# Optimization experiments

Measured on AMD Instinct MI355X. Metric: run time of the kernel, lower is better.

The kernel has to match this reference:

```python
import jax, jax.numpy as jnp
import numpy as np

B, N, F, H, OUT, K, L = 32, 2048, 3, 64, 128, 16, 3


def _edge_mlp(e, w1, b1, wo, bo):
    # Faithful to the given MLP.forward: layer1 -> ReLU -> output (layer2 is skipped!)
    return jax.nn.relu(e @ w1 + b1) @ wo + bo


def _dynamic_edge_conv(x, k, w1, b1, wo, bo):
    # x: [B, N, D]. kNN in feature space (self included, distance 0), per graph.
    sq = jnp.sum(x * x, axis=-1)                                   # [B, N]
    d2 = sq[:, :, None] + sq[:, None, :] - 2.0 * jnp.einsum('bnd,bmd->bnm', x, x)
    _, idx = jax.lax.top_k(-d2, k)                                 # [B, N, K]
    x_j = jax.vmap(lambda xb, ib: xb[ib])(x, idx)                  # [B, N, K, D] gather
    x_i = jnp.broadcast_to(x[:, :, None, :], x_j.shape)
    e = jnp.concatenate([x_i, x_j - x_i], axis=-1)                 # EdgeConv message [B,N,K,2D]
    h = _edge_mlp(e, w1, b1, wo, bo)                               # [B, N, K, H]
    return jnp.mean(h, axis=2)                                     # aggr='mean' -> [B, N, H]


def setup_inputs() -> dict:
    key = jax.random.key(0)
    ks = jax.random.split(key, 20)
    inp = {'x': jax.random.normal(ks[0], (B, N, F), dtype=jnp.float32)}
    kit = iter(ks[1:])
    for i in range(L):
        din = 2 * F if i == 0 else 2 * H
        inp[f'w1_{i}'] = jax.random.normal(next(kit), (din, H), jnp.float32) / np.sqrt(din)
        inp[f'b1_{i}'] = jnp.zeros((H,), jnp.float32)
        inp[f'wo_{i}'] = jax.random.normal(next(kit), (H, H), jnp.float32) / np.sqrt(H)
        inp[f'bo_{i}'] = jnp.zeros((H,), jnp.float32)
    inp['fw1'] = jax.random.normal(next(kit), (H, H), jnp.float32) / np.sqrt(H)
    inp['fb1'] = jnp.zeros((H,), jnp.float32)
    inp['fw2'] = jax.random.normal(next(kit), (H, OUT), jnp.float32) / np.sqrt(H)
    inp['fb2'] = jnp.zeros((OUT,), jnp.float32)
    return inp


def reference(x, w1_0, b1_0, wo_0, bo_0, w1_1, b1_1, wo_1, bo_1, w1_2, b1_2, wo_2, bo_2, fw1, fb1, fw2, fb2):
    layers = [(w1_0, b1_0, wo_0, bo_0), (w1_1, b1_1, wo_1, bo_1), (w1_2, b1_2, wo_2, bo_2)]
    h = x
    for (w1, b1, wo, bo) in layers:
        h = _dynamic_edge_conv(h, K, w1, b1, wo, bo)
    g = jnp.mean(h, axis=1)                                        # global_mean_pool -> [B, H]
    return jax.nn.relu(g @ fw1 + fb1) @ fw2 + fb2                  # [B, OUT]
```

## Files before the change

kernel.cpp:

```cpp
#include <hip/hip_runtime.h>

#define BB 32
#define NN 2048
#define FF 3
#define HH 64
#define OUTC 128
#define KK 16
#define BN (BB * NN)

typedef __attribute__((ext_vector_type(8))) __bf16 bf16x8;
typedef __attribute__((ext_vector_type(4))) float f32x4;

__device__ __forceinline__ unsigned int packkey(float d2, unsigned int m) {
    unsigned int bb = __builtin_bit_cast(unsigned int, d2);
    unsigned int msk = (unsigned int)((int)bb >> 31);
    unsigned int srt = bb ^ (msk | 0x80000000u);
    return (srt & 0xFFFFF800u) | m;
}

__device__ __forceinline__ void ce(unsigned int& a, unsigned int& b) {
    unsigned int lo = a < b ? a : b;
    unsigned int hi = a < b ? b : a;
    a = lo; b = hi;
}

__device__ __forceinline__ void sort16(unsigned int k[16]) {
#pragma unroll
    for (int p = 1; p < 16; p <<= 1)
#pragma unroll
        for (int q = p; q >= 1; q >>= 1)
#pragma unroll
            for (int j = q % p; j + q < 16; j += 2 * q)
#pragma unroll
                for (int i = 0; i < q; ++i) {
                    int x = i + j, y = i + j + q;
                    if (y < 16 && (x / (2 * p) == y / (2 * p))) ce(k[x], k[y]);
                }
}

__device__ __forceinline__ void merge16(unsigned int keys[16], const unsigned int nk[16]) {
    unsigned int t[16];
#pragma unroll
    for (int i = 0; i < 16; ++i) {
        unsigned int b = nk[15 - i];
        t[i] = keys[i] < b ? keys[i] : b;
    }
#pragma unroll
    for (int d = 8; d >= 1; d >>= 1)
#pragma unroll
        for (int i = 0; i < 16; ++i)
            if ((i & d) == 0) ce(t[i], t[i ^ d]);
#pragma unroll
    for (int i = 0; i < 16; ++i) keys[i] = t[i];
}

__device__ __forceinline__ unsigned short bfbits(float v) {
    return __builtin_bit_cast(unsigned short, (__bf16)v);
}

__global__ __launch_bounds__(256) void pack3_kernel(const float* __restrict__ x,
                                                    const float* __restrict__ w1,
                                                    const float* __restrict__ b1,
                                                    float* __restrict__ P,
                                                    float* __restrict__ Q,
                                                    unsigned short* __restrict__ idx32) {
    __shared__ float4 lds_c[256];
    __shared__ unsigned int Km[64 * 68];
    const int tid = threadIdx.x;

    if (blockIdx.x >= 1024) {
        const int h = tid & 63;
        const int pl = tid >> 6;
        const long p = (long)(blockIdx.x - 1024) * 4 + pl;
        const float* fp = x + p * 3;
        const float fv[3] = {fp[0], fp[1], fp[2]};
        float accp = 0.f, accq = 0.f;
#pragma unroll
        for (int d = 0; d < 3; ++d) {
            float wa = w1[d * HH + h];
            float wb = w1[(3 + d) * HH + h];
            accp = fmaf(fv[d], wa - wb, accp);
            accq = fmaf(fv[d], wb, accq);
        }
        P[p * HH + h] = accp + b1[h];
        Q[p * HH + h] = accq;
        return;
    }

    const int xcd = blockIdx.x & 7;
    const int ii = blockIdx.x >> 3;
    const int b = xcd + 8 * (ii >> 5);
    const int rg = ii & 31;
    const long pbase = (long)b * NN;
    const int r = tid >> 2, slot = tid & 3;
    const int row = rg * 64 + r;

    const float* rp = x + (pbase + row) * 3;
    const float xr0 = rp[0], xr1 = rp[1], xr2 = rp[2];

    unsigned int keys[KK];
#pragma unroll
    for (int j = 0; j < KK; ++j) keys[j] = 0xFFFFFFFFu;

    float c0, c1, c2, c3;
    {
        const float* cp = x + (pbase + tid) * 3;
        c0 = cp[0]; c1 = cp[1]; c2 = cp[2];
        c3 = c0 * c0 + c1 * c1 + c2 * c2;
    }

    for (int t = 0; t < NN / 256; ++t) {
        __syncthreads();
        lds_c[tid] = make_float4(c0, c1, c2, c3);
        __syncthreads();
        if (t < NN / 256 - 1) {
            const int m = (t + 1) * 256 + tid;
            const float* cp = x + (pbase + m) * 3;
            c0 = cp[0]; c1 = cp[1]; c2 = cp[2];
            c3 = c0 * c0 + c1 * c1 + c2 * c2;
        }
        const int cbase = slot * 64;
#pragma unroll
        for (int bb = 0; bb < 4; ++bb) {
            unsigned int nk[16];
#pragma unroll
            for (int cc = 0; cc < 16; ++cc) {
                float4 v = lds_c[cbase + bb * 16 + cc];
                float dot = fmaf(xr0, v.x, fmaf(xr1, v.y, xr2 * v.z));
                float d2 = fmaf(-2.0f, dot, v.w);
                nk[cc] = packkey(d2, (unsigned int)(t * 256 + cbase + bb * 16 + cc));
            }
            sort16(nk);
            merge16(keys, nk);
        }
    }

    {
        uint4* kw = (uint4*)&Km[r * 68 + slot * 16];
#pragma unroll
        for (int q = 0; q < 4; ++q)
            kw[q] = make_uint4(keys[4 * q], keys[4 * q + 1], keys[4 * q + 2], keys[4 * q + 3]);
    }
    __syncthreads();
    if (slot < 2) {
        const unsigned int* k0 = &Km[r * 68 + slot * 32];
        const unsigned int* k1 = k0 + 16;
        unsigned short ms[16];
#pragma unroll
        for (int j = 0; j < 16; ++j) {
            unsigned int a = k0[j], bv = k1[15 - j];
            ms[j] = (unsigned short)((a < bv ? a : bv) & 0x7FFu);
        }
        uint4* op = (uint4*)(idx32 + ((pbase + row) * 32 + slot * 16));
        op[0] = ((const uint4*)ms)[0];
        op[1] = ((const uint4*)ms)[1];
    }
}

__global__ __launch_bounds__(256) void prep_pq64_kernel(const float* __restrict__ feat,
                                                        const float* __restrict__ w1,
                                                        const float* __restrict__ b1,
                                                        float* __restrict__ P,
                                                        float* __restrict__ Q,
                                                        float* __restrict__ sqo) {
    __shared__ float rows[64 * HH];
    const int tid = threadIdx.x;
    const int h = tid & 63;
    const int wv = tid >> 6;
    const long row0 = (long)blockIdx.x * 64;

    float wdiff[64], wbv[64];
#pragma unroll
    for (int d = 0; d < 64; ++d) {
        float wa = w1[d * HH + h];
        float wb_ = w1[(HH + d) * HH + h];
        wdiff[d] = wa - wb_;
        wbv[d] = wb_;
    }
    const float bv = b1[h];

    {
        const float4* src = (const float4*)(feat + row0 * HH);
        float4* dst = (float4*)rows;
#pragma unroll
        for (int i = 0; i < 4; ++i) dst[tid + 256 * i] = src[tid + 256 * i];
    }
    __syncthreads();

    for (int r = wv * 16; r < wv * 16 + 16; ++r) {
        const long p = row0 + r;
        if (sqo) {
            float fvh = rows[r * HH + h];
            float s = fvh * fvh;
            s += __shfl_xor(s, 1);
            s += __shfl_xor(s, 2);
            s += __shfl_xor(s, 4);
            s += __shfl_xor(s, 8);
            s += __shfl_xor(s, 16);
            s += __shfl_xor(s, 32);
            if (h == 0) sqo[p] = s;
        }
        float ap0 = 0.f, ap1 = 0.f, aq0 = 0.f, aq1 = 0.f;
#pragma unroll
        for (int d4 = 0; d4 < 16; ++d4) {
            float4 fv = *(const float4*)&rows[r * HH + d4 * 4];
            ap0 = fmaf(fv.x, wdiff[4 * d4 + 0], ap0);
            aq0 = fmaf(fv.x, wbv[4 * d4 + 0], aq0);
            ap1 = fmaf(fv.y, wdiff[4 * d4 + 1], ap1);
            aq1 = fmaf(fv.y, wbv[4 * d4 + 1], aq1);
            ap0 = fmaf(fv.z, wdiff[4 * d4 + 2], ap0);
            aq0 = fmaf(fv.z, wbv[4 * d4 + 2], aq0);
            ap1 = fmaf(fv.w, wdiff[4 * d4 + 3], ap1);
            aq1 = fmaf(fv.w, wbv[4 * d4 + 3], aq1);
        }
        P[p * HH + h] = (ap0 + ap1) + bv;
        Q[p * HH + h] = aq0 + aq1;
    }
}

#define APAD 80
#define DPAD 68

__global__ __launch_bounds__(256) void knn_filter_kernel(const float* __restrict__ feat,
                                                         const float* __restrict__ sq,
                                                         unsigned short* __restrict__ idx32) {
    __shared__ __align__(16) __bf16 Ab[64 * APAD];
    __shared__ __align__(16) __bf16 Bb[64 * APAD];
    __shared__ __align__(16) unsigned int Dt[64 * DPAD];
    __shared__ float SqC[64];

    const int tid = threadIdx.x;
    const int xcd = blockIdx.x & 7;
    const int ii = blockIdx.x >> 3;
    const int b = xcd + 8 * (ii >> 5);
    const int rg = ii & 31;
    const long pbase = (long)b * NN;
    const int row0 = rg * 64;

    {
        const float4* src = (const float4*)(feat + (pbase + row0) * 64);
#pragma unroll
        for (int it = 0; it < 4; ++it) {
            const int i = it * 256 + tid;
            float4 v = src[i];
            const int rw = i >> 4, col = (i & 15) * 4;
            unsigned short u[4] = {bfbits(v.x), bfbits(v.y), bfbits(v.z), bfbits(v.w)};
            *(uint2*)&Ab[rw * APAD + col] = *(const uint2*)u;
        }
    }
    __syncthreads();

    const int wv = tid >> 6, ln = tid & 63;
    const int n16 = ln & 15, quad = ln >> 4;
    bf16x8 af0, af1;
    {
        const __bf16* ap = &Ab[(wv * 16 + n16) * APAD + quad * 8];
        af0 = *(const bf16x8*)ap;
        af1 = *(const bf16x8*)(ap + 32);
    }

    const int r = tid >> 2, slot = tid & 3;
    unsigned int keys[KK];
#pragma unroll
    for (int j = 0; j < KK; ++j) keys[j] = 0xFFFFFFFFu;

    float4 pv[4];
    float psq;
    {
        const float4* src = (const float4*)(feat + pbase * 64);
#pragma unroll
        for (int it = 0; it < 4; ++it) pv[it] = src[it * 256 + tid];
        psq = (tid < 64) ? sq[pbase + tid] : 0.f;
    }

    for (int t = 0; t < NN / 64; ++t) {
#pragma unroll
        for (int it = 0; it < 4; ++it) {
            const int i = it * 256 + tid;
            const int rw = i >> 4, col = (i & 15) * 4;
            unsigned short u[4] = {bfbits(pv[it].x), bfbits(pv[it].y),
                                   bfbits(pv[it].z), bfbits(pv[it].w)};
            *(uint2*)&Bb[rw * APAD + col] = *(const uint2*)u;
        }
        if (tid < 64) SqC[tid] = psq;
        __syncthreads();

#pragma unroll
        for (int ct = 0; ct < 4; ++ct) {
            const __bf16* bp = &Bb[(ct * 16 + n16) * APAD + quad * 8];
            bf16x8 bf0 = *(const bf16x8*)bp;
            bf16x8 bf1 = *(const bf16x8*)(bp + 32);
            f32x4 acc = {0.f, 0.f, 0.f, 0.f};
            acc = __builtin_amdgcn_mfma_f32_16x16x32_bf16(af0, bf0, acc, 0, 0, 0);
            acc = __builtin_amdgcn_mfma_f32_16x16x32_bf16(af1, bf1, acc, 0, 0, 0);
            const int ccol = ct * 16 + n16;
            const float sqc = SqC[ccol];
            const unsigned int m = (unsigned int)(t * 64 + ccol);
#pragma unroll
            for (int rr = 0; rr < 4; ++rr) {
                const int rrow = wv * 16 + quad * 4 + rr;
                Dt[rrow * DPAD + ccol] = packkey(fmaf(-2.0f, acc[rr], sqc), m);
            }
        }
        __syncthreads();

        if (t < NN / 64 - 1) {
            const float4* src = (const float4*)(feat + (pbase + (long)(t + 1) * 64) * 64);
#pragma unroll
            for (int it = 0; it < 4; ++it) pv[it] = src[it * 256 + tid];
            if (tid < 64) psq = sq[pbase + (t + 1) * 64 + tid];
        }

        {
            const uint4* kp = (const uint4*)&Dt[r * DPAD + slot * 16];
            unsigned int nk[16];
#pragma unroll
            for (int q = 0; q < 4; ++q) {
                uint4 kv = kp[q];
                nk[4 * q + 0] = kv.x; nk[4 * q + 1] = kv.y;
                nk[4 * q + 2] = kv.z; nk[4 * q + 3] = kv.w;
            }
            sort16(nk);
            merge16(keys, nk);
        }
    }

    __syncthreads();
    {
        uint4* kw = (uint4*)&Dt[r * DPAD + slot * 16];
#pragma unroll
        for (int q = 0; q < 4; ++q)
            kw[q] = make_uint4(keys[4 * q], keys[4 * q + 1], keys[4 * q + 2], keys[4 * q + 3]);
    }
    __syncthreads();
    if (slot < 2) {
        const unsigned int* k0 = &Dt[r * DPAD + slot * 32];
        const unsigned int* k1 = k0 + 16;
        unsigned short ms[16];
#pragma unroll
        for (int j = 0; j < 16; ++j) {
            unsigned int a = k0[j], bv = k1[15 - j];
            ms[j] = (unsigned short)((a < bv ? a : bv) & 0x7FFu);
        }
        uint4* op = (uint4*)(idx32 + ((pbase + row0 + r) * 32 + slot * 16));
        op[0] = ((const uint4*)ms)[0];
        op[1] = ((const uint4*)ms)[1];
    }
}

__global__ __launch_bounds__(256) void rescore3_kernel(const float* __restrict__ x,
                                                       const unsigned short* __restrict__ idx32,
                                                       const float* __restrict__ P,
                                                       const float* __restrict__ Q,
                                                       const float* __restrict__ wo,
                                                       const float* __restrict__ bo,
                                                       float* __restrict__ outf,
                                                       float* __restrict__ sqn) {
    __shared__ float rowf[8][3];
    __shared__ float Sc[8][32];
    __shared__ int Ji[8][32];
    __shared__ int Li[8][KK];
    __shared__ float Rl[8][HH];
    const int tid = threadIdx.x;
    const int w = tid >> 6, ln = tid & 63;
    const int rw = ln >> 5, c = ln & 31;
    const int xcd = blockIdx.x & 7;
    const int ii = blockIdx.x >> 3;
    const int batch = xcd + 8 * (ii >> 8);
    const int rb = ii & 255;
    const long pbase = (long)batch * NN;
    const long pblk = pbase + (long)rb * 8;
    const long p = pblk + w * 2 + rw;
    const int row_ = w * 2 + rw;

    for (int i = tid; i < 24; i += 256) rowf[i / 3][i % 3] = x[pblk * 3 + i];
    Ji[row_][c] = (int)idx32[p * 32 + c];
    __syncthreads();

    {
        const int jj = Ji[row_][c];
        const float* cp = x + (pbase + jj) * 3;
        const float c0 = cp[0], c1 = cp[1], c2 = cp[2];
        const float sqc = c0 * c0 + c1 * c1 + c2 * c2;
        float dot = fmaf(rowf[row_][0], c0, fmaf(rowf[row_][1], c1, rowf[row_][2] * c2));
        Sc[row_][c] = fmaf(-2.0f, dot, sqc);
    }
    __syncthreads();

    {
        const float score = Sc[row_][c];
        const int j = Ji[row_][c];
        int rank = 0;
#pragma unroll
        for (int m = 0; m < 32; ++m) {
            float dm = Sc[row_][m];
            int jm = Ji[row_][m];
            rank += (dm < score || (dm == score && jm < j)) ? 1 : 0;
        }
        if (rank < KK) Li[row_][rank] = j;
    }
    __syncthreads();

    const int h = tid & 63, pl = tid >> 6;
#pragma unroll
    for (int rr0 = 0; rr0 < 2; ++rr0) {
        const int rr = pl + rr0 * 4;
        const long pp = pblk + rr;
        const float Pv = P[pp * HH + h];
        float acc = 0.f;
#pragma unroll
        for (int k = 0; k < KK; ++k) {
            int j2 = Li[rr][k];
            acc += fmaxf(Pv + Q[(pbase + j2) * HH + h], 0.f);
        }
        Rl[rr][h] = acc * (1.f / KK);
    }
    __syncthreads();
#pragma unroll
    for (int rr0 = 0; rr0 < 2; ++rr0) {
        const int rr = pl + rr0 * 4;
        float o = bo[h];
#pragma unroll
        for (int l = 0; l < HH; ++l) o = fmaf(Rl[rr][l], wo[l * HH + h], o);
        outf[(pblk + rr) * HH + h] = o;
        float s2 = o * o;
        s2 += __shfl_xor(s2, 1);
        s2 += __shfl_xor(s2, 2);
        s2 += __shfl_xor(s2, 4);
        s2 += __shfl_xor(s2, 8);
        s2 += __shfl_xor(s2, 16);
        s2 += __shfl_xor(s2, 32);
        if (h == 0) sqn[pblk + rr] = s2;
    }
}

__global__ __launch_bounds__(256) void rescore64_kernel(const float* __restrict__ feat,
                                                        const float* __restrict__ sq,
                                                        const unsigned short* __restrict__ idx32,
                                                        const float* __restrict__ P,
                                                        const float* __restrict__ Q,
                                                        const float* __restrict__ wo,
                                                        const float* __restrict__ bo,
                                                        float* __restrict__ outf) {
    __shared__ float rowf[8][HH];
    __shared__ float Sc[8][32];
    __shared__ int Ji[8][32];
    __shared__ float Sq32[8][32];
    __shared__ int Li[8][KK];
    __shared__ float Rl[8][HH];
    const int tid = threadIdx.x;
    const int w = tid >> 6, ln = tid & 63;
    const int rw = ln >> 5, c = ln & 31;
    const int xcd = blockIdx.x & 7;
    const int ii = blockIdx.x >> 3;
    const int batch = xcd + 8 * (ii >> 8);
    const int rb = ii & 255;
    const long pbase = (long)batch * NN;
    const long pblk = pbase + (long)rb * 8;
    const long p = pblk + w * 2 + rw;
    const int row_ = w * 2 + rw;

    for (int i = tid; i < 8 * HH; i += 256) rowf[i / HH][i % HH] = feat[pblk * HH + i];
    {
        const int j0 = (int)idx32[p * 32 + c];
        Ji[row_][c] = j0;
        Sq32[row_][c] = sq[pbase + j0];
    }
    __syncthreads();

    {
        const int cg = ln >> 2, e = ln & 3;
#pragma unroll
        for (int rr = 0; rr < 2; ++rr) {
#pragma unroll
            for (int pp = 0; pp < 2; ++pp) {
                const int row = w * 2 + rr;
                const int cand = pp * 16 + cg;
                const int jj = Ji[row][cand];
                const float* cb = feat + (pbase + jj) * 64;
                float part = 0.f;
#pragma unroll
                for (int blk = 0; blk < 4; ++blk) {
                    float4 cv = *(const float4*)(cb + blk * 16 + e * 4);
                    float4 rv = *(const float4*)&rowf[row][blk * 16 + e * 4];
                    part = fmaf(rv.x, cv.x, part);
                    part = fmaf(rv.y, cv.y, part);
                    part = fmaf(rv.z, cv.z, part);
                    part = fmaf(rv.w, cv.w, part);
                }
                part += __shfl_xor(part, 1);
                part += __shfl_xor(part, 2);
                if (e == 0) Sc[row][cand] = fmaf(-2.0f, part, Sq32[row][cand]);
            }
        }
    }
    __syncthreads();

    {
        const float score = Sc[row_][c];
        const int j = Ji[row_][c];
        int rank = 0;
#pragma unroll
        for (int m = 0; m < 32; ++m) {
            float dm = Sc[row_][m];
            int jm = Ji[row_][m];
            rank += (dm < score || (dm == score && jm < j)) ? 1 : 0;
        }
        if (rank < KK) Li[row_][rank] = j;
    }
    __syncthreads();

    const int h = tid & 63, pl = tid >> 6;
#pragma unroll
    for (int rr0 = 0; rr0 < 2; ++rr0) {
        const int rr = pl + rr0 * 4;
        const long pp = pblk + rr;
        const float Pv = P[pp * HH + h];
        float acc = 0.f;
#pragma unroll
        for (int k = 0; k < KK; ++k) {
            int j2 = Li[rr][k];
            acc += fmaxf(Pv + Q[(pbase + j2) * HH + h], 0.f);
        }
        Rl[rr][h] = acc * (1.f / KK);
    }
    __syncthreads();
#pragma unroll
    for (int rr0 = 0; rr0 < 2; ++rr0) {
        const int rr = pl + rr0 * 4;
        float o = bo[h];
#pragma unroll
        for (int l = 0; l < HH; ++l) o = fmaf(Rl[rr][l], wo[l * HH + h], o);
        outf[(pblk + rr) * HH + h] = o;
    }
}

__global__ __launch_bounds__(256) void pool_partial_kernel(const float* __restrict__ feat,
                                                           float* __restrict__ pp) {
    __shared__ float part[4][HH];
    const int batch = blockIdx.x >> 3;
    const int chk = blockIdx.x & 7;
    const int tid = threadIdx.x;
    const int h = tid & 63;
    const int sub = tid >> 6;
    float s = 0.f;
    const float* fp = feat + ((long)batch * NN + chk * 256 + sub * 64) * HH + h;
    for (int n = 0; n < 64; ++n) s += fp[(long)n * HH];
    part[sub][h] = s;
    __syncthreads();
    if (tid < HH)
        pp[(batch * 8 + chk) * HH + h] = part[0][h] + part[1][h] + part[2][h] + part[3][h];
}

__global__ __launch_bounds__(256) void head_kernel(const float* __restrict__ pp,
                                                   const float* __restrict__ fw1,
                                                   const float* __restrict__ fb1,
                                                   const float* __restrict__ fw2,
                                                   const float* __restrict__ fb2,
                                                   float* __restrict__ out) {
    __shared__ float g[HH];
    __shared__ float tl[HH];
    const int b = blockIdx.x;
    const int tid = threadIdx.x;
    if (tid < HH) {
        float s = 0.f;
#pragma unroll
        for (int c = 0; c < 8; ++c) s += pp[(b * 8 + c) * HH + tid];
        g[tid] = s * (1.f / NN);
    }
    __syncthreads();
    if (tid < HH) {
        float a = fb1[tid];
#pragma unroll
        for (int l = 0; l < HH; ++l) a = fmaf(g[l], fw1[l * HH + tid], a);
        tl[tid] = fmaxf(a, 0.f);
    }
    __syncthreads();
    if (tid < OUTC) {
        float o = fb2[tid];
#pragma unroll
        for (int l = 0; l < HH; ++l) o = fmaf(tl[l], fw2[l * OUTC + tid], o);
        out[(long)b * OUTC + tid] = o;
    }
}

extern "C" void kernel_launch(void* const* d_in, const int* in_sizes, int n_in,
                              void* d_out, int out_size, void* d_ws, size_t ws_size,
                              hipStream_t stream) {
    const float* x    = (const float*)d_in[0];
    const float* w1_0 = (const float*)d_in[1];
    const float* b1_0 = (const float*)d_in[2];
    const float* wo_0 = (const float*)d_in[3];
    const float* bo_0 = (const float*)d_in[4];
    const float* w1_1 = (const float*)d_in[5];
    const float* b1_1 = (const float*)d_in[6];
    const float* wo_1 = (const float*)d_in[7];
    const float* bo_1 = (const float*)d_in[8];
    const float* w1_2 = (const float*)d_in[9];
    const float* b1_2 = (const float*)d_in[10];
    const float* wo_2 = (const float*)d_in[11];
    const float* bo_2 = (const float*)d_in[12];
    const float* fw1  = (const float*)d_in[13];
    const float* fb1  = (const float*)d_in[14];
    const float* fw2  = (const float*)d_in[15];
    const float* fb2  = (const float*)d_in[16];
    float* out = (float*)d_out;

    float* featA = (float*)d_ws;
    float* featB = featA + (long)BN * HH;
    float* Pb    = featB + (long)BN * HH;
    float* Qb    = Pb + (long)BN * HH;
    float* sqA   = Qb + (long)BN * HH;
    float* sqB   = sqA + BN;
    unsigned short* idx32 = (unsigned short*)(sqB + BN);
    float* ppb   = (float*)(idx32 + (long)BN * 32);

    pack3_kernel<<<1024 + BN / 4, 256, 0, stream>>>(x, w1_0, b1_0, Pb, Qb, idx32);
    rescore3_kernel<<<BN / 8, 256, 0, stream>>>(x, idx32, Pb, Qb, wo_0, bo_0, featA, sqB);

    prep_pq64_kernel<<<BN / 64, 256, 0, stream>>>(featA, w1_1, b1_1, Pb, Qb, nullptr);
    knn_filter_kernel<<<BB * 32, 256, 0, stream>>>(featA, sqB, idx32);
    rescore64_kernel<<<BN / 8, 256, 0, stream>>>(featA, sqB, idx32, Pb, Qb, wo_1, bo_1, featB);

    prep_pq64_kernel<<<BN / 64, 256, 0, stream>>>(featB, w1_2, b1_2, Pb, Qb, sqA);
    knn_filter_kernel<<<BB * 32, 256, 0, stream>>>(featB, sqA, idx32);
    rescore64_kernel<<<BN / 8, 256, 0, stream>>>(featB, sqA, idx32, Pb, Qb, wo_2, bo_2, featA);

    pool_partial_kernel<<<BB * 8, 256, 0, stream>>>(featA, ppb);
    head_kernel<<<BB, 256, 0, stream>>>(ppb, fw1, fb1, fw2, fb2, out);
}
```

Measured before the change: 619.2 us.

## Merge P/Q prep into kNN filter launch and fold squared norms into rescore

The separate prep_pq64 and knn_filter kernels are merged into one launch of 2048 blocks. Blocks 0-1023 run the kNN filter and blocks 1024-2047 compute P/Q, sharing one union shared-memory buffer, so the two independent jobs overlap on the GPU and one launch plus its tail is removed. The squared-norm computation for the next layer moves out of prep and into the rescore epilogue, which avoids re-reading the features. Rescore also gets a min-blocks-per-SM launch bound and loads P early. In exchange, the union buffer makes every block reserve the larger shared-memory footprint, and the launch bound may increase register pressure.

```diff
diff --git a/kernel.cpp b/kernel.cpp
--- a/kernel.cpp
+++ b/kernel.cpp
@@ -157,79 +157,70 @@
     }
 }
 
-__global__ __launch_bounds__(256) void prep_pq64_kernel(const float* __restrict__ feat,
-                                                        const float* __restrict__ w1,
-                                                        const float* __restrict__ b1,
-                                                        float* __restrict__ P,
-                                                        float* __restrict__ Q,
-                                                        float* __restrict__ sqo) {
-    __shared__ float rows[64 * HH];
-    const int tid = threadIdx.x;
-    const int h = tid & 63;
-    const int wv = tid >> 6;
-    const long row0 = (long)blockIdx.x * 64;
-
-    float wdiff[64], wbv[64];
-#pragma unroll
-    for (int d = 0; d < 64; ++d) {
-        float wa = w1[d * HH + h];
-        float wb_ = w1[(HH + d) * HH + h];
-        wdiff[d] = wa - wb_;
-        wbv[d] = wb_;
-    }
-    const float bv = b1[h];
-
-    {
-        const float4* src = (const float4*)(feat + row0 * HH);
-        float4* dst = (float4*)rows;
-#pragma unroll
-        for (int i = 0; i < 4; ++i) dst[tid + 256 * i] = src[tid + 256 * i];
-    }
-    __syncthreads();
-
-    for (int r = wv * 16; r < wv * 16 + 16; ++r) {
-        const long p = row0 + r;
-        if (sqo) {
-            float fvh = rows[r * HH + h];
-            float s = fvh * fvh;
-            s += __shfl_xor(s, 1);
-            s += __shfl_xor(s, 2);
-            s += __shfl_xor(s, 4);
-            s += __shfl_xor(s, 8);
-            s += __shfl_xor(s, 16);
-            s += __shfl_xor(s, 32);
-            if (h == 0) sqo[p] = s;
-        }
-        float ap0 = 0.f, ap1 = 0.f, aq0 = 0.f, aq1 = 0.f;
-#pragma unroll
-        for (int d4 = 0; d4 < 16; ++d4) {
-            float4 fv = *(const float4*)&rows[r * HH + d4 * 4];
-            ap0 = fmaf(fv.x, wdiff[4 * d4 + 0], ap0);
-            aq0 = fmaf(fv.x, wbv[4 * d4 + 0], aq0);
-            ap1 = fmaf(fv.y, wdiff[4 * d4 + 1], ap1);
-            aq1 = fmaf(fv.y, wbv[4 * d4 + 1], aq1);
-            ap0 = fmaf(fv.z, wdiff[4 * d4 + 2], ap0);
-            aq0 = fmaf(fv.z, wbv[4 * d4 + 2], aq0);
-            ap1 = fmaf(fv.w, wdiff[4 * d4 + 3], ap1);
-            aq1 = fmaf(fv.w, wbv[4 * d4 + 3], aq1);
-        }
-        P[p * HH + h] = (ap0 + ap1) + bv;
-        Q[p * HH + h] = aq0 + aq1;
-    }
-}
-
 #define APAD 80
 #define DPAD 68
-
-__global__ __launch_bounds__(256) void knn_filter_kernel(const float* __restrict__ feat,
-                                                         const float* __restrict__ sq,
-                                                         unsigned short* __restrict__ idx32) {
-    __shared__ __align__(16) __bf16 Ab[64 * APAD];
-    __shared__ __align__(16) __bf16 Bb[64 * APAD];
-    __shared__ __align__(16) unsigned int Dt[64 * DPAD];
-    __shared__ float SqC[64];
-
+#define SMEM_U32 (38144 / 4)
+
+__global__ __launch_bounds__(256) void filter_prep64_kernel(const float* __restrict__ feat,
+                                                            const float* __restrict__ sq,
+                                                            const float* __restrict__ w1,
+                                                            const float* __restrict__ b1,
+                                                            float* __restrict__ P,
+                                                            float* __restrict__ Q,
+                                                            unsigned short* __restrict__ idx32) {
+    __shared__ __align__(16) unsigned int smem[SMEM_U32];
     const int tid = threadIdx.x;
+
+    if (blockIdx.x >= 1024) {
+        float* rows = (float*)smem;
+        const int h = tid & 63;
+        const int wv = tid >> 6;
+        const long row0 = (long)(blockIdx.x - 1024) * 64;
+
+        float wdiff[64], wbv[64];
+#pragma unroll
+        for (int d = 0; d < 64; ++d) {
+            float wa = w1[d * HH + h];
+            float wb_ = w1[(HH + d) * HH + h];
+            wdiff[d] = wa - wb_;
+            wbv[d] = wb_;
+        }
+        const float bv = b1[h];
+
+        {
+            const float4* src = (const float4*)(feat + row0 * HH);
+            float4* dst = (float4*)rows;
+#pragma unroll
+            for (int i = 0; i < 4; ++i) dst[tid + 256 * i] = src[tid + 256 * i];
+        }
+        __syncthreads();
+
+        for (int r = wv * 16; r < wv * 16 + 16; ++r) {
+            const long p = row0 + r;
+            float ap0 = 0.f, ap1 = 0.f, aq0 = 0.f, aq1 = 0.f;
+#pragma unroll
+            for (int d4 = 0; d4 < 16; ++d4) {
+                float4 fv = *(const float4*)&rows[r * HH + d4 * 4];
+                ap0 = fmaf(fv.x, wdiff[4 * d4 + 0], ap0);
+                aq0 = fmaf(fv.x, wbv[4 * d4 + 0], aq0);
+                ap1 = fmaf(fv.y, wdiff[4 * d4 + 1], ap1);
+                aq1 = fmaf(fv.y, wbv[4 * d4 + 1], aq1);
+                ap0 = fmaf(fv.z, wdiff[4 * d4 + 2], ap0);
+                aq0 = fmaf(fv.z, wbv[4 * d4 + 2], aq0);
+                ap1 = fmaf(fv.w, wdiff[4 * d4 + 3], ap1);
+                aq1 = fmaf(fv.w, wbv[4 * d4 + 3], aq1);
+            }
+            P[p * HH + h] = (ap0 + ap1) + bv;
+            Q[p * HH + h] = aq0 + aq1;
+        }
+        return;
+    }
+
+    __bf16* Ab = (__bf16*)smem;
+    __bf16* Bb = Ab + 64 * APAD;
+    unsigned int* Dt = (unsigned int*)(Bb + 64 * APAD);
+    float* SqC = (float*)(Dt + 64 * DPAD);
+
     const int xcd = blockIdx.x & 7;
     const int ii = blockIdx.x >> 3;
     const int b = xcd + 8 * (ii >> 5);
@@ -434,14 +425,15 @@
     }
 }
 
-__global__ __launch_bounds__(256) void rescore64_kernel(const float* __restrict__ feat,
-                                                        const float* __restrict__ sq,
-                                                        const unsigned short* __restrict__ idx32,
-                                                        const float* __restrict__ P,
-                                                        const float* __restrict__ Q,
-                                                        const float* __restrict__ wo,
-                                                        const float* __restrict__ bo,
-                                                        float* __restrict__ outf) {
+__global__ __launch_bounds__(256, 8) void rescore64_kernel(const float* __restrict__ feat,
+                                                           const float* __restrict__ sq,
+                                                           const unsigned short* __restrict__ idx32,
+                                                           const float* __restrict__ P,
+                                                           const float* __restrict__ Q,
+                                                           const float* __restrict__ wo,
+                                                           const float* __restrict__ bo,
+                                                           float* __restrict__ outf,
+                                                           float* __restrict__ sqn) {
     __shared__ float rowf[8][HH];
     __shared__ float Sc[8][32];
     __shared__ int Ji[8][32];
@@ -459,6 +451,10 @@
     const long pblk = pbase + (long)rb * 8;
     const long p = pblk + w * 2 + rw;
     const int row_ = w * 2 + rw;
+    const int h = tid & 63, pl = tid >> 6;
+
+    const float Pv0 = P[(pblk + pl) * HH + h];
+    const float Pv1 = P[(pblk + pl + 4) * HH + h];
 
     for (int i = tid; i < 8 * HH; i += 256) rowf[i / HH][i % HH] = feat[pblk * HH + i];
     {
@@ -510,12 +506,10 @@
     }
     __syncthreads();
 
-    const int h = tid & 63, pl = tid >> 6;
 #pragma unroll
     for (int rr0 = 0; rr0 < 2; ++rr0) {
         const int rr = pl + rr0 * 4;
-        const long pp = pblk + rr;
-        const float Pv = P[pp * HH + h];
+        const float Pv = rr0 ? Pv1 : Pv0;
         float acc = 0.f;
 #pragma unroll
         for (int k = 0; k < KK; ++k) {
@@ -532,6 +526,16 @@
 #pragma unroll
         for (int l = 0; l < HH; ++l) o = fmaf(Rl[rr][l], wo[l * HH + h], o);
         outf[(pblk + rr) * HH + h] = o;
+        if (sqn) {
+            float s2 = o * o;
+            s2 += __shfl_xor(s2, 1);
+            s2 += __shfl_xor(s2, 2);
+            s2 += __shfl_xor(s2, 4);
+            s2 += __shfl_xor(s2, 8);
+            s2 += __shfl_xor(s2, 16);
+            s2 += __shfl_xor(s2, 32);
+            if (h == 0) sqn[pblk + rr] = s2;
+        }
     }
 }
 
@@ -618,13 +622,13 @@
     pack3_kernel<<<1024 + BN / 4, 256, 0, stream>>>(x, w1_0, b1_0, Pb, Qb, idx32);
     rescore3_kernel<<<BN / 8, 256, 0, stream>>>(x, idx32, Pb, Qb, wo_0, bo_0, featA, sqB);
 
-    prep_pq64_kernel<<<BN / 64, 256, 0, stream>>>(featA, w1_1, b1_1, Pb, Qb, nullptr);
-    knn_filter_kernel<<<BB * 32, 256, 0, stream>>>(featA, sqB, idx32);
-    rescore64_kernel<<<BN / 8, 256, 0, stream>>>(featA, sqB, idx32, Pb, Qb, wo_1, bo_1, featB);
-
-    prep_pq64_kernel<<<BN / 64, 256, 0, stream>>>(featB, w1_2, b1_2, Pb, Qb, sqA);
-    knn_filter_kernel<<<BB * 32, 256, 0, stream>>>(featB, sqA, idx32);
-    rescore64_kernel<<<BN / 8, 256, 0, stream>>>(featB, sqA, idx32, Pb, Qb, wo_2, bo_2, featA);
+    filter_prep64_kernel<<<2048, 256, 0, stream>>>(featA, sqB, w1_1, b1_1, Pb, Qb, idx32);
+    rescore64_kernel<<<BN / 8, 256, 0, stream>>>(featA, sqB, idx32, Pb, Qb, wo_1, bo_1,
+                                                 featB, sqA);
+
+    filter_prep64_kernel<<<2048, 256, 0, stream>>>(featB, sqA, w1_2, b1_2, Pb, Qb, idx32);
+    rescore64_kernel<<<BN / 8, 256, 0, stream>>>(featB, sqA, idx32, Pb, Qb, wo_2, bo_2,
+                                                 featA, nullptr);
 
     pool_partial_kernel<<<BB * 8, 256, 0, stream>>>(featA, ppb);
     head_kernel<<<BB, 256, 0, stream>>>(ppb, fw1, fb1, fw2, fb2, out);
```

Result: slower. 1.027 ms (+65.9%).
